# Optimization experiments

Measured on AMD Instinct MI355X. Metric: run time of the kernel, lower is better.

The kernel has to match this reference:

```python
import jax, jax.numpy as jnp
import numpy as np

B, C, N, D, F = 2048, 64, 64, 64, 128  # batch, cin_hidden, num_features, embed_dim, feature_maps


def setup_inputs() -> dict:
    key = jax.random.key(0)
    k1, k2, k3 = jax.random.split(key, 3)
    xj = jax.random.normal(k1, (B, C, D), dtype=jnp.float32)
    x0 = jax.random.normal(k2, (B, N, D), dtype=jnp.float32)
    # xavier_uniform_ on (F, C, N): fan_in = C*N? torch treats dim1 as fan_in-ish;
    # exact init distribution is irrelevant for correctness testing, use scaled uniform.
    limit = float(np.sqrt(6.0 / (C + N)))
    W = jax.random.uniform(k3, (F, C, N), dtype=jnp.float32, minval=-limit, maxval=limit)
    return {"xj": xj, "x0": x0, "W": W}


def reference(xj, x0, W):
    # Original: hadamard[b,c,n,d] = x0[b,n,d]*xj[b,c,d];
    # out[b,f,c,d] = sum_n hadamard * W[f,c,n]; cin_out = sum_c out; cin_p_out = sum_d cin_out.
    # Fused: cin_out[b,f,d] = sum_{c,n} W[f,c,n] * xj[b,c,d] * x0[b,n,d]
    cin_out = jnp.einsum('bcd,bnd,fcn->bfd', xj, x0, W)  # (B, F, D)
    cin_p_out = jnp.sum(cin_out, axis=-1)  # (B, F)
    return (cin_out, cin_p_out)
```

## Files before the change

kernel.cpp:

```cpp
#include <hip/hip_runtime.h>


typedef _Float16 f16;
typedef __attribute__((ext_vector_type(8))) _Float16 half8;
typedef __attribute__((ext_vector_type(16))) float f32x16;
typedef __attribute__((ext_vector_type(4))) float f32x4;

#define MFMA(a, b, c) __builtin_amdgcn_mfma_f32_32x32x16_f16(a, b, c, 0, 0, 0)

union U8 { half8 v; unsigned u[4]; };

__device__ __forceinline__ half8 scale8a(half8 a, unsigned hdup) {
  U8 in, out;
  in.v = a;
  asm("v_pk_mul_f16 %0, %1, %2" : "=v"(out.u[0]) : "v"(in.u[0]), "v"(hdup));
  asm("v_pk_mul_f16 %0, %1, %2" : "=v"(out.u[1]) : "v"(in.u[1]), "v"(hdup));
  asm("v_pk_mul_f16 %0, %1, %2" : "=v"(out.u[2]) : "v"(in.u[2]), "v"(hdup));
  asm("v_pk_mul_f16 %0, %1, %2" : "=v"(out.u[3]) : "v"(in.u[3]), "v"(hdup));
  return out.v;
}

__device__ __forceinline__ unsigned dup16(float f) {
  f16 h = (f16)f;
  union { f16 h; unsigned short s; } u; u.h = h;
  return (unsigned)u.s * 0x10001u;
}

__global__ __launch_bounds__(256) void wscat_kernel(const float* __restrict__ W,
                                                    f16* __restrict__ Wb) {
  const int tid = blockIdx.x * 256 + threadIdx.x;
  const int c = tid >> 10, s = tid & 1023;
  const int gk = s >> 6, ln = s & 63;
  const int g = gk >> 2, kk = gk & 3, hi = ln >> 5, lr = ln & 31;
  const int f = g * 32 + lr, n0 = kk * 16 + hi * 8;
  const float* src = W + (size_t)f * 4096 + c * 64 + n0;
  const float4 a = *(const float4*)src;
  const float4 b = *(const float4*)(src + 4);
  half8 r;
  r[0] = (f16)a.x; r[1] = (f16)a.y; r[2] = (f16)a.z; r[3] = (f16)a.w;
  r[4] = (f16)b.x; r[5] = (f16)b.y; r[6] = (f16)b.z; r[7] = (f16)b.w;
  *(half8*)(Wb + (size_t)c * 8192 + s * 8) = r;
}

__global__ __launch_bounds__(256, 2) void cin_kernel(
    const float* __restrict__ xj, const float* __restrict__ x0,
    const f16* __restrict__ Wb, float* __restrict__ out,
    float* __restrict__ pout) {
  __shared__ f16 x0T[2 * 4096];
  __shared__ unsigned xjD[2 * 4096];

  const int t = threadIdx.x;
  const int wid = t >> 6, lane = t & 63;
  const int b0 = blockIdx.x * 2;

#pragma unroll
  for (int bb = 0; bb < 2; ++bb) {
    const float* s0 = x0 + (size_t)(b0 + bb) * 4096;
    const float* sj = xj + (size_t)(b0 + bb) * 4096;
    {
      const int n = lane, d0 = wid * 16;
      const int chb = n >> 3, sub = n & 7;
#pragma unroll
      for (int q = 0; q < 4; ++q) {
        const float4 v = *(const float4*)(s0 + n * 64 + d0 + q * 4);
#pragma unroll
        for (int j = 0; j < 4; ++j) {
          const int d = d0 + q * 4 + j;
          x0T[bb * 4096 + d * 64 + ((chb ^ (d & 7)) << 3) + sub] =
              (f16)(((const float*)&v)[j]);
        }
      }
    }
#pragma unroll
    for (int p = 0; p < 4; ++p) {
      const int e = p * 1024 + t * 4;
      const float4 v = *(const float4*)(sj + e);
      unsigned* dst = &xjD[bb * 4096 + e];
      dst[0] = dup16(v.x); dst[1] = dup16(v.y);
      dst[2] = dup16(v.z); dst[3] = dup16(v.w);
    }
  }
  __syncthreads();

  const int wg = wid;
  const int lr = lane & 31, hi = lane >> 5;

  half8 af[4][4];
#pragma unroll
  for (int mf = 0; mf < 4; ++mf) {
    const int bb = mf >> 1;
    const int d = (mf & 1) * 32 + lr;
#pragma unroll
    for (int kk = 0; kk < 4; ++kk)
      af[mf][kk] = *(const half8*)&x0T[bb * 4096 + d * 64 +
                                       (((kk * 2 + hi) ^ (d & 7)) << 3)];
  }

  f32x16 accE[4] = {};
  f32x16 accO[4] = {};

  const half8* wp = (const half8*)Wb + wg * 256 + lane;
  const unsigned* xjA = &xjD[lr];
  const unsigned* xjB = &xjD[lr] + 64;

  half8 wA0 = wp[0],    wA1 = wp[64],        wA2 = wp[128],        wA3 = wp[192];
  half8 wB0 = wp[1024], wB1 = wp[1024 + 64], wB2 = wp[1024 + 128], wB3 = wp[1024 + 192];
  unsigned xA0 = xjA[0], xA1 = xjA[32], xA2 = xjA[4096], xA3 = xjA[4096 + 32];
  unsigned xB0 = xjB[0], xB1 = xjB[32], xB2 = xjB[4096], xB3 = xjB[4096 + 32];

  const half8* wpA = wp + 2048;
  const half8* wpB = wp + 3072;
  const unsigned* xjpA = xjA + 128;
  const unsigned* xjpB = xjB + 128;

#pragma unroll 1
  for (int cc = 0; cc < 32; ++cc) {
    __builtin_amdgcn_s_setprio(1);
#pragma unroll
    for (int kk = 0; kk < 4; ++kk) {
      const half8 wa = (kk == 0) ? wA0 : (kk == 1) ? wA1 : (kk == 2) ? wA2 : wA3;
      const half8 wb = (kk == 0) ? wB0 : (kk == 1) ? wB1 : (kk == 2) ? wB2 : wB3;
      accE[0] = MFMA(scale8a(af[0][kk], xA0), wa, accE[0]);
      accE[1] = MFMA(scale8a(af[1][kk], xA1), wa, accE[1]);
      accE[2] = MFMA(scale8a(af[2][kk], xA2), wa, accE[2]);
      accE[3] = MFMA(scale8a(af[3][kk], xA3), wa, accE[3]);
      accO[0] = MFMA(scale8a(af[0][kk], xB0), wb, accO[0]);
      accO[1] = MFMA(scale8a(af[1][kk], xB1), wb, accO[1]);
      accO[2] = MFMA(scale8a(af[2][kk], xB2), wb, accO[2]);
      accO[3] = MFMA(scale8a(af[3][kk], xB3), wb, accO[3]);
    }
    __builtin_amdgcn_s_setprio(0);
    if (cc < 31) {
      wA0 = wpA[0]; wA1 = wpA[64]; wA2 = wpA[128]; wA3 = wpA[192];
      xA0 = xjpA[0]; xA1 = xjpA[32]; xA2 = xjpA[4096]; xA3 = xjpA[4096 + 32];
      wpA += 2048; xjpA += 128;
      wB0 = wpB[0]; wB1 = wpB[64]; wB2 = wpB[128]; wB3 = wpB[192];
      xB0 = xjpB[0]; xB1 = xjpB[32]; xB2 = xjpB[4096]; xB3 = xjpB[4096 + 32];
      wpB += 2048; xjpB += 128;
    }
  }

  const int fcol = wg * 32 + lr;
  float ps[4];
#pragma unroll
  for (int mf = 0; mf < 4; ++mf) {
    const int b = b0 + (mf >> 1);
    float* ob = out + (size_t)b * 8192 + (size_t)fcol * 64 + (mf & 1) * 32;
    const f32x16 v = accE[mf] + accO[mf];
    float s = 0.f;
#pragma unroll
    for (int q = 0; q < 4; ++q) {
      f32x4 vv = { v[4 * q], v[4 * q + 1], v[4 * q + 2], v[4 * q + 3] };
      *(f32x4*)(ob + q * 8 + hi * 4) = vv;
      s += vv[0] + vv[1] + vv[2] + vv[3];
    }
    ps[mf] = s;
  }
  float pA = ps[0] + ps[1];
  float pB = ps[2] + ps[3];
  pA += __shfl_xor(pA, 32, 64);
  pB += __shfl_xor(pB, 32, 64);
  if (hi == 0) {
    pout[(size_t)b0 * 128 + fcol] = pA;
    pout[(size_t)(b0 + 1) * 128 + fcol] = pB;
  }
}

extern "C" void kernel_launch(void* const* d_in, const int* in_sizes, int n_in,
                              void* d_out, int out_size, void* d_ws, size_t ws_size,
                              hipStream_t stream) {
  const float* xj = (const float*)d_in[0];
  const float* x0 = (const float*)d_in[1];
  const float* W  = (const float*)d_in[2];
  float* out  = (float*)d_out;
  float* pout = out + (size_t)2048 * 128 * 64;
  f16* Wb = (f16*)d_ws;

  wscat_kernel<<<256, 256, 0, stream>>>(W, Wb);
  cin_kernel<<<1024, 256, 0, stream>>>(xj, x0, Wb, out, pout);
}
```

Before: 147.6 us.

## Single accumulator set, per-wave rotated channel order, interleaved weight prefetch

Merges the even/odd accumulator sets into one, which frees 64 VGPRs per lane. Each wave now starts its channel loop at a different offset (wg*16, wrapping mod 64), so the four waves stream different weight slices at the same moment. Each weight register is reloaded right after its last MFMA use, spreading the global loads through the MFMA stream instead of issuing them in a block at the end of the iteration. The trade-off is that one accumulator chain doubles the MFMA dependency length, and the wraparound prefetch on the last iteration loads data that is never used.

Measured after the change: 143.8 us. 1.03x faster.

```diff
diff --git a/kernel.cpp b/kernel.cpp
--- a/kernel.cpp
+++ b/kernel.cpp
@@ -96,48 +96,77 @@
                                        (((kk * 2 + hi) ^ (d & 7)) << 3)];
   }
 
-  f32x16 accE[4] = {};
-  f32x16 accO[4] = {};
-
-  const half8* wp = (const half8*)Wb + wg * 256 + lane;
-  const unsigned* xjA = &xjD[lr];
-  const unsigned* xjB = &xjD[lr] + 64;
-
-  half8 wA0 = wp[0],    wA1 = wp[64],        wA2 = wp[128],        wA3 = wp[192];
-  half8 wB0 = wp[1024], wB1 = wp[1024 + 64], wB2 = wp[1024 + 128], wB3 = wp[1024 + 192];
-  unsigned xA0 = xjA[0], xA1 = xjA[32], xA2 = xjA[4096], xA3 = xjA[4096 + 32];
-  unsigned xB0 = xjB[0], xB1 = xjB[32], xB2 = xjB[4096], xB3 = xjB[4096 + 32];
-
-  const half8* wpA = wp + 2048;
-  const half8* wpB = wp + 3072;
-  const unsigned* xjpA = xjA + 128;
-  const unsigned* xjpB = xjB + 128;
+  f32x16 acc[4] = {};
+
+  const half8* wbase = (const half8*)Wb + wg * 256 + lane;
+  const unsigned* xbase = &xjD[lr];
+
+  const int c0 = wg * 16;
+
+  const half8* pA0 = wbase + c0 * 1024;
+  const half8* pB0 = wbase + (c0 + 1) * 1024;
+  half8 wA0 = pA0[0], wA1 = pA0[64], wA2 = pA0[128], wA3 = pA0[192];
+  half8 wB0 = pB0[0], wB1 = pB0[64], wB2 = pB0[128], wB3 = pB0[192];
+  const unsigned* xA = xbase + c0 * 64;
+  const unsigned* xB = xbase + (c0 + 1) * 64;
+  unsigned xA0 = xA[0], xA1 = xA[32], xA2 = xA[4096], xA3 = xA[4096 + 32];
+  unsigned xB0 = xB[0], xB1 = xB[32], xB2 = xB[4096], xB3 = xB[4096 + 32];
 
 #pragma unroll 1
   for (int cc = 0; cc < 32; ++cc) {
+    const int cEn = (c0 + 2 * cc + 2) & 63;
+    const half8* pAn = wbase + cEn * 1024;
+    const half8* pBn = pAn + 1024;
+    const unsigned* xAn = xbase + cEn * 64;
+    const unsigned* xBn = xAn + 64;
+
     __builtin_amdgcn_s_setprio(1);
-#pragma unroll
-    for (int kk = 0; kk < 4; ++kk) {
-      const half8 wa = (kk == 0) ? wA0 : (kk == 1) ? wA1 : (kk == 2) ? wA2 : wA3;
-      const half8 wb = (kk == 0) ? wB0 : (kk == 1) ? wB1 : (kk == 2) ? wB2 : wB3;
-      accE[0] = MFMA(scale8a(af[0][kk], xA0), wa, accE[0]);
-      accE[1] = MFMA(scale8a(af[1][kk], xA1), wa, accE[1]);
-      accE[2] = MFMA(scale8a(af[2][kk], xA2), wa, accE[2]);
-      accE[3] = MFMA(scale8a(af[3][kk], xA3), wa, accE[3]);
-      accO[0] = MFMA(scale8a(af[0][kk], xB0), wb, accO[0]);
-      accO[1] = MFMA(scale8a(af[1][kk], xB1), wb, accO[1]);
-      accO[2] = MFMA(scale8a(af[2][kk], xB2), wb, accO[2]);
-      accO[3] = MFMA(scale8a(af[3][kk], xB3), wb, accO[3]);
-    }
+    acc[0] = MFMA(scale8a(af[0][0], xA0), wA0, acc[0]);
+    acc[1] = MFMA(scale8a(af[1][0], xA1), wA0, acc[1]);
+    acc[2] = MFMA(scale8a(af[2][0], xA2), wA0, acc[2]);
+    acc[3] = MFMA(scale8a(af[3][0], xA3), wA0, acc[3]);
+    wA0 = pAn[0];
+    acc[0] = MFMA(scale8a(af[0][1], xA0), wA1, acc[0]);
+    acc[1] = MFMA(scale8a(af[1][1], xA1), wA1, acc[1]);
+    acc[2] = MFMA(scale8a(af[2][1], xA2), wA1, acc[2]);
+    acc[3] = MFMA(scale8a(af[3][1], xA3), wA1, acc[3]);
+    wA1 = pAn[64];
+    acc[0] = MFMA(scale8a(af[0][2], xA0), wA2, acc[0]);
+    acc[1] = MFMA(scale8a(af[1][2], xA1), wA2, acc[1]);
+    acc[2] = MFMA(scale8a(af[2][2], xA2), wA2, acc[2]);
+    acc[3] = MFMA(scale8a(af[3][2], xA3), wA2, acc[3]);
+    wA2 = pAn[128];
+    acc[0] = MFMA(scale8a(af[0][3], xA0), wA3, acc[0]);
+    acc[1] = MFMA(scale8a(af[1][3], xA1), wA3, acc[1]);
+    acc[2] = MFMA(scale8a(af[2][3], xA2), wA3, acc[2]);
+    acc[3] = MFMA(scale8a(af[3][3], xA3), wA3, acc[3]);
+    wA3 = pAn[192];
     __builtin_amdgcn_s_setprio(0);
-    if (cc < 31) {
-      wA0 = wpA[0]; wA1 = wpA[64]; wA2 = wpA[128]; wA3 = wpA[192];
-      xA0 = xjpA[0]; xA1 = xjpA[32]; xA2 = xjpA[4096]; xA3 = xjpA[4096 + 32];
-      wpA += 2048; xjpA += 128;
-      wB0 = wpB[0]; wB1 = wpB[64]; wB2 = wpB[128]; wB3 = wpB[192];
-      xB0 = xjpB[0]; xB1 = xjpB[32]; xB2 = xjpB[4096]; xB3 = xjpB[4096 + 32];
-      wpB += 2048; xjpB += 128;
-    }
+    xA0 = xAn[0]; xA1 = xAn[32]; xA2 = xAn[4096]; xA3 = xAn[4096 + 32];
+
+    __builtin_amdgcn_s_setprio(1);
+    acc[0] = MFMA(scale8a(af[0][0], xB0), wB0, acc[0]);
+    acc[1] = MFMA(scale8a(af[1][0], xB1), wB0, acc[1]);
+    acc[2] = MFMA(scale8a(af[2][0], xB2), wB0, acc[2]);
+    acc[3] = MFMA(scale8a(af[3][0], xB3), wB0, acc[3]);
+    wB0 = pBn[0];
+    acc[0] = MFMA(scale8a(af[0][1], xB0), wB1, acc[0]);
+    acc[1] = MFMA(scale8a(af[1][1], xB1), wB1, acc[1]);
+    acc[2] = MFMA(scale8a(af[2][1], xB2), wB1, acc[2]);
+    acc[3] = MFMA(scale8a(af[3][1], xB3), wB1, acc[3]);
+    wB1 = pBn[64];
+    acc[0] = MFMA(scale8a(af[0][2], xB0), wB2, acc[0]);
+    acc[1] = MFMA(scale8a(af[1][2], xB1), wB2, acc[1]);
+    acc[2] = MFMA(scale8a(af[2][2], xB2), wB2, acc[2]);
+    acc[3] = MFMA(scale8a(af[3][2], xB3), wB2, acc[3]);
+    wB2 = pBn[128];
+    acc[0] = MFMA(scale8a(af[0][3], xB0), wB3, acc[0]);
+    acc[1] = MFMA(scale8a(af[1][3], xB1), wB3, acc[1]);
+    acc[2] = MFMA(scale8a(af[2][3], xB2), wB3, acc[2]);
+    acc[3] = MFMA(scale8a(af[3][3], xB3), wB3, acc[3]);
+    wB3 = pBn[192];
+    __builtin_amdgcn_s_setprio(0);
+    xB0 = xBn[0]; xB1 = xBn[32]; xB2 = xBn[4096]; xB3 = xBn[4096 + 32];
   }
 
   const int fcol = wg * 32 + lr;
@@ -146,7 +175,7 @@
   for (int mf = 0; mf < 4; ++mf) {
     const int b = b0 + (mf >> 1);
     float* ob = out + (size_t)b * 8192 + (size_t)fcol * 64 + (mf & 1) * 32;
-    const f32x16 v = accE[mf] + accO[mf];
+    const f32x16 v = acc[mf];
     float s = 0.f;
 #pragma unroll
     for (int q = 0; q < 4; ++q) {
```

## Retile CIN waves over batch and F halves with interleaved W prefetch

Applied to the files above, without the earlier changes.

Each wave now owns one batch and a 64-wide F half (2x2 MFMA tiles) instead of 32 F columns across both batches. This halves the x0 A-fragments per wave and makes each scaled A operand feed two MFMAs. The c loop runs 63 iterations with per-kk W loads interleaved between MFMAs rather than batched at the end, plus a peeled final iteration. It drops the even/odd split accumulators and setprio, so each MFMA chain now depends on the previous one with less independence to hide latency, and W reuse per wave changes from two batches to one.

Measured after the change: 165.3 us. 1.12x slower.

```diff
diff --git a/kernel.cpp b/kernel.cpp
--- a/kernel.cpp
+++ b/kernel.cpp
@@ -82,87 +82,109 @@
   }
   __syncthreads();
 
-  const int wg = wid;
+  const int bb = wid >> 1, fh = wid & 1;
   const int lr = lane & 31, hi = lane >> 5;
 
-  half8 af[4][4];
-#pragma unroll
-  for (int mf = 0; mf < 4; ++mf) {
-    const int bb = mf >> 1;
-    const int d = (mf & 1) * 32 + lr;
+  half8 af[2][4];
+#pragma unroll
+  for (int mf = 0; mf < 2; ++mf) {
+    const int d = mf * 32 + lr;
 #pragma unroll
     for (int kk = 0; kk < 4; ++kk)
       af[mf][kk] = *(const half8*)&x0T[bb * 4096 + d * 64 +
                                        (((kk * 2 + hi) ^ (d & 7)) << 3)];
   }
 
-  f32x16 accE[4] = {};
-  f32x16 accO[4] = {};
-
-  const half8* wp = (const half8*)Wb + wg * 256 + lane;
-  const unsigned* xjA = &xjD[lr];
-  const unsigned* xjB = &xjD[lr] + 64;
-
-  half8 wA0 = wp[0],    wA1 = wp[64],        wA2 = wp[128],        wA3 = wp[192];
-  half8 wB0 = wp[1024], wB1 = wp[1024 + 64], wB2 = wp[1024 + 128], wB3 = wp[1024 + 192];
-  unsigned xA0 = xjA[0], xA1 = xjA[32], xA2 = xjA[4096], xA3 = xjA[4096 + 32];
-  unsigned xB0 = xjB[0], xB1 = xjB[32], xB2 = xjB[4096], xB3 = xjB[4096 + 32];
-
-  const half8* wpA = wp + 2048;
-  const half8* wpB = wp + 3072;
-  const unsigned* xjpA = xjA + 128;
-  const unsigned* xjpB = xjB + 128;
+  f32x16 acc00 = {}, acc01 = {}, acc10 = {}, acc11 = {};
+
+  const half8* wp = (const half8*)Wb + fh * 512 + lane;
+
+  half8 w00 = wp[0],   w01 = wp[64],  w02 = wp[128], w03 = wp[192];
+  half8 w10 = wp[256], w11 = wp[320], w12 = wp[384], w13 = wp[448];
+  const half8* wpn = wp + 1024;
+
+  const unsigned* xjp = &xjD[bb * 4096 + lr];
+  unsigned x0v = xjp[0], x1v = xjp[32];
+  const unsigned* xjpn = xjp + 64;
 
 #pragma unroll 1
-  for (int cc = 0; cc < 32; ++cc) {
-    __builtin_amdgcn_s_setprio(1);
-#pragma unroll
-    for (int kk = 0; kk < 4; ++kk) {
-      const half8 wa = (kk == 0) ? wA0 : (kk == 1) ? wA1 : (kk == 2) ? wA2 : wA3;
-      const half8 wb = (kk == 0) ? wB0 : (kk == 1) ? wB1 : (kk == 2) ? wB2 : wB3;
-      accE[0] = MFMA(scale8a(af[0][kk], xA0), wa, accE[0]);
-      accE[1] = MFMA(scale8a(af[1][kk], xA1), wa, accE[1]);
-      accE[2] = MFMA(scale8a(af[2][kk], xA2), wa, accE[2]);
-      accE[3] = MFMA(scale8a(af[3][kk], xA3), wa, accE[3]);
-      accO[0] = MFMA(scale8a(af[0][kk], xB0), wb, accO[0]);
-      accO[1] = MFMA(scale8a(af[1][kk], xB1), wb, accO[1]);
-      accO[2] = MFMA(scale8a(af[2][kk], xB2), wb, accO[2]);
-      accO[3] = MFMA(scale8a(af[3][kk], xB3), wb, accO[3]);
+  for (int c = 0; c < 63; ++c) {
+    const unsigned xn0 = xjpn[0], xn1 = xjpn[32];
+
+    half8 a0 = scale8a(af[0][0], x0v);
+    half8 a1 = scale8a(af[1][0], x1v);
+    acc00 = MFMA(a0, w00, acc00);
+    acc10 = MFMA(a1, w00, acc10);
+    w00 = wpn[0];
+    acc01 = MFMA(a0, w10, acc01);
+    acc11 = MFMA(a1, w10, acc11);
+    w10 = wpn[256];
+    a0 = scale8a(af[0][1], x0v);
+    a1 = scale8a(af[1][1], x1v);
+    acc00 = MFMA(a0, w01, acc00);
+    acc10 = MFMA(a1, w01, acc10);
+    w01 = wpn[64];
+    acc01 = MFMA(a0, w11, acc01);
+    acc11 = MFMA(a1, w11, acc11);
+    w11 = wpn[320];
+    a0 = scale8a(af[0][2], x0v);
+    a1 = scale8a(af[1][2], x1v);
+    acc00 = MFMA(a0, w02, acc00);
+    acc10 = MFMA(a1, w02, acc10);
+    w02 = wpn[128];
+    acc01 = MFMA(a0, w12, acc01);
+    acc11 = MFMA(a1, w12, acc11);
+    w12 = wpn[384];
+    a0 = scale8a(af[0][3], x0v);
+    a1 = scale8a(af[1][3], x1v);
+    acc00 = MFMA(a0, w03, acc00);
+    acc10 = MFMA(a1, w03, acc10);
+    w03 = wpn[192];
+    acc01 = MFMA(a0, w13, acc01);
+    acc11 = MFMA(a1, w13, acc11);
+    w13 = wpn[448];
+
+    x0v = xn0; x1v = xn1;
+    wpn += 1024; xjpn += 64;
+  }
+
+#pragma unroll
+  for (int kk = 0; kk < 4; ++kk) {
+    const half8 a0 = scale8a(af[0][kk], x0v);
+    const half8 a1 = scale8a(af[1][kk], x1v);
+    const half8 wl = (kk == 0) ? w00 : (kk == 1) ? w01 : (kk == 2) ? w02 : w03;
+    const half8 wh = (kk == 0) ? w10 : (kk == 1) ? w11 : (kk == 2) ? w12 : w13;
+    acc00 = MFMA(a0, wl, acc00);
+    acc10 = MFMA(a1, wl, acc10);
+    acc01 = MFMA(a0, wh, acc01);
+    acc11 = MFMA(a1, wh, acc11);
+  }
+
+  const int b = b0 + bb;
+  float psum[2] = {0.f, 0.f};
+#pragma unroll
+  for (int nf = 0; nf < 2; ++nf) {
+    const int fcol = fh * 64 + nf * 32 + lr;
+    float* ob = out + (size_t)b * 8192 + (size_t)fcol * 64;
+#pragma unroll
+    for (int mf = 0; mf < 2; ++mf) {
+      const f32x16 v = (nf == 0) ? ((mf == 0) ? acc00 : acc10)
+                                 : ((mf == 0) ? acc01 : acc11);
+      float s = 0.f;
+#pragma unroll
+      for (int q = 0; q < 4; ++q) {
+        f32x4 vv = { v[4 * q], v[4 * q + 1], v[4 * q + 2], v[4 * q + 3] };
+        *(f32x4*)(ob + mf * 32 + q * 8 + hi * 4) = vv;
+        s += vv[0] + vv[1] + vv[2] + vv[3];
+      }
+      psum[nf] += s;
     }
-    __builtin_amdgcn_s_setprio(0);
-    if (cc < 31) {
-      wA0 = wpA[0]; wA1 = wpA[64]; wA2 = wpA[128]; wA3 = wpA[192];
-      xA0 = xjpA[0]; xA1 = xjpA[32]; xA2 = xjpA[4096]; xA3 = xjpA[4096 + 32];
-      wpA += 2048; xjpA += 128;
-      wB0 = wpB[0]; wB1 = wpB[64]; wB2 = wpB[128]; wB3 = wpB[192];
-      xB0 = xjpB[0]; xB1 = xjpB[32]; xB2 = xjpB[4096]; xB3 = xjpB[4096 + 32];
-      wpB += 2048; xjpB += 128;
-    }
-  }
-
-  const int fcol = wg * 32 + lr;
-  float ps[4];
-#pragma unroll
-  for (int mf = 0; mf < 4; ++mf) {
-    const int b = b0 + (mf >> 1);
-    float* ob = out + (size_t)b * 8192 + (size_t)fcol * 64 + (mf & 1) * 32;
-    const f32x16 v = accE[mf] + accO[mf];
-    float s = 0.f;
-#pragma unroll
-    for (int q = 0; q < 4; ++q) {
-      f32x4 vv = { v[4 * q], v[4 * q + 1], v[4 * q + 2], v[4 * q + 3] };
-      *(f32x4*)(ob + q * 8 + hi * 4) = vv;
-      s += vv[0] + vv[1] + vv[2] + vv[3];
-    }
-    ps[mf] = s;
-  }
-  float pA = ps[0] + ps[1];
-  float pB = ps[2] + ps[3];
-  pA += __shfl_xor(pA, 32, 64);
-  pB += __shfl_xor(pB, 32, 64);
-  if (hi == 0) {
-    pout[(size_t)b0 * 128 + fcol] = pA;
-    pout[(size_t)(b0 + 1) * 128 + fcol] = pB;
+  }
+#pragma unroll
+  for (int nf = 0; nf < 2; ++nf) {
+    float s = psum[nf];
+    s += __shfl_xor(s, 32, 64);
+    if (hi == 0) pout[(size_t)b * 128 + fh * 64 + nf * 32 + lr] = s;
   }
 }
 
```
